# Performance work log

Hardware: AMD Instinct MI355X
Metric: run time of the kernel (lower is better)

## Reference

```python
import jax, jax.numpy as jnp
import numpy as np

NEG_SLOPE = 0.15
MASK_VAL = -1e9


def setup_inputs() -> dict:
    key = jax.random.key(0)
    k1, k2, k3, k4, k5 = jax.random.split(key, 5)
    B, N, D, H, QKV = 4, 1024, 128, 8, 16
    h = jax.random.normal(k1, (B, N, D), dtype=jnp.float32)
    same_cluster = jax.random.randint(k2, (B, N, N), 0, 2) > 0
    # nn.Linear weights stored as [in, out] (x @ W); scaled like default init
    Wa = jax.random.normal(k3, (2 * D + 1, H), dtype=jnp.float32) / np.sqrt(2 * D + 1)
    Wv = jax.random.normal(k4, (D, H * QKV), dtype=jnp.float32) / np.sqrt(D)
    Wo = jax.random.normal(k5, (H * QKV, D), dtype=jnp.float32) / np.sqrt(H * QKV)
    return {"h": h, "same_cluster": same_cluster, "Wa": Wa, "Wv": Wv, "Wo": Wo, "local_only": 0}


def reference(h, same_cluster, Wa, Wv, Wo, local_only):
    B, N, D = h.shape
    H = Wa.shape[1]
    # concat([hi, hj, edge]) @ Wa == hi @ Wa[:D] + hj @ Wa[D:2D] + edge * Wa[2D]
    Wa_i, Wa_j, w_e = Wa[:D], Wa[D:2 * D], Wa[2 * D]  # [D,H], [D,H], [H]
    s_i = h @ Wa_i  # [B, N, H]
    s_j = h @ Wa_j  # [B, N, H]
    edge = same_cluster.astype(h.dtype)  # [B, N, N]
    scores = s_i[:, :, None, :] + s_j[:, None, :, :] + edge[..., None] * w_e  # [B,N,N,H]
    scores = jax.nn.leaky_relu(scores, negative_slope=NEG_SLOPE)
    scores = jnp.moveaxis(scores, -1, 1)  # [B, H, N, N]
    if local_only:
        scores = jnp.where(same_cluster[:, None, :, :], scores, MASK_VAL)
    alpha = jax.nn.softmax(scores, axis=-1)  # [B, H, N, N]
    v = (h @ Wv).reshape(B, N, H, -1).transpose(0, 2, 1, 3)  # [B, H, N, qkv]
    out = jnp.einsum('bhij,bhjd->bhid', alpha, v)  # [B, H, N, qkv]
    out = out.transpose(0, 2, 1, 3).reshape(B, N, -1)  # [B, N, H*qkv]
    return out @ Wo  # [B, N, D]
```

## Files before the change

### kernel.cpp

```cpp
#include <hip/hip_runtime.h>
#include <hip/hip_bf16.h>


#define NEG_SLOPE 0.15f
#define B_ 4
#define N_ 1024
#define D_ 128
#define H_ 8
#define QKV_ 16
#define BN_ (B_ * N_)

__global__ __launch_bounds__(256) void prep_kernel(
    const float* __restrict__ h, const float* __restrict__ Wa,
    const float* __restrict__ Wv, float* __restrict__ SIt,
    float* __restrict__ SJt, float* __restrict__ V)
{
    __shared__ float hl[8][128];
    const int t  = threadIdx.x;
    const int R0 = blockIdx.x * 8;

    {
        const int f = t * 4;
        *(float4*)(&hl[0][0] + f) = *(const float4*)(h + R0 * 128 + f);
    }
    __syncthreads();

    const int cq = t & 31, rq = t >> 5;
    const int c4 = cq * 4;
    float acc0 = 0.f, acc1 = 0.f, acc2 = 0.f, acc3 = 0.f;
    #pragma unroll 8
    for (int k = 0; k < 128; ++k) {
        const float4 w = *(const float4*)(Wv + k * 128 + c4);
        const float a = hl[rq][k];
        acc0 += a * w.x; acc1 += a * w.y; acc2 += a * w.z; acc3 += a * w.w;
    }
    {
        const int R = R0 + rq, b = R >> 10, n = R & 1023;
        const int head = cq >> 2, dd = (cq & 3) * 4;
        float4 o; o.x = acc0; o.y = acc1; o.z = acc2; o.w = acc3;
        *(float4*)(V + ((size_t)(b * H_ + head) * N_ + n) * QKV_ + dd) = o;
    }

    {
        const int task = t >> 1, half = t & 1;
        const int row = task >> 4, which = (task >> 3) & 1, hh = task & 7;
        const float* wcol = Wa + which * 128 * H_ + hh;
        float s = 0.f;
        #pragma unroll 8
        for (int kk = 0; kk < 64; ++kk) {
            const int k = half * 64 + kk;
            s += hl[row][k] * wcol[k * H_];
        }
        s += __shfl_xor(s, 1, 64);
        if (!half) {
            float* dst = which ? SJt : SIt;
            dst[hh * BN_ + R0 + row] = s;
        }
    }
}

__global__ __launch_bounds__(256, 4) void attn_kernel(
    const float* __restrict__ SIt, const float* __restrict__ SJt,
    const float* __restrict__ V, const int* __restrict__ edge,
    const float* __restrict__ Wa, const int* __restrict__ local_only,
    float* __restrict__ ATT)
{
    const int t  = threadIdx.x;
    const int w  = t >> 6;
    const int l  = t & 63;
    const int hh = blockIdx.y;
    const int b  = blockIdx.z;
    const int i0 = blockIdx.x * 16 + w * 4;
    const int bn0 = b * N_;

    const float we = Wa[2 * D_ * H_ + hh];
    const int   lo = local_only[0];

    float si[4];
    #pragma unroll
    for (int r = 0; r < 4; ++r) si[r] = SIt[hh * BN_ + bn0 + i0 + r];

    const float* vbase  = V + (size_t)(b * H_ + hh) * N_ * QKV_;
    const float* sjbase = SJt + hh * BN_ + bn0;
    const int*   ebase  = edge + (size_t)(bn0 + i0) * N_;

    float acc[4][16];
    #pragma unroll
    for (int r = 0; r < 4; ++r)
        #pragma unroll
        for (int d = 0; d < 16; ++d) acc[r][d] = 0.f;
    float dsum[4] = {0.f, 0.f, 0.f, 0.f};

    #pragma unroll 2
    for (int j0 = 0; j0 < N_; j0 += 64) {
        const int j = j0 + l;
        const float sj = sjbase[j];
        const float4* vp = (const float4*)(vbase + j * QKV_);
        const float4 v0 = vp[0], v1 = vp[1], v2 = vp[2], v3 = vp[3];
        int e[4];
        #pragma unroll
        for (int r = 0; r < 4; ++r) e[r] = ebase[r * N_ + j];

        #pragma unroll
        for (int r = 0; r < 4; ++r) {
            float sc = si[r] + sj + (e[r] ? we : 0.f);
            sc = fmaxf(sc, NEG_SLOPE * sc);
            float p = __expf(sc);
            if (lo && !e[r]) p = 0.f;
            dsum[r] += p;
            acc[r][0]  += p * v0.x; acc[r][1]  += p * v0.y;
            acc[r][2]  += p * v0.z; acc[r][3]  += p * v0.w;
            acc[r][4]  += p * v1.x; acc[r][5]  += p * v1.y;
            acc[r][6]  += p * v1.z; acc[r][7]  += p * v1.w;
            acc[r][8]  += p * v2.x; acc[r][9]  += p * v2.y;
            acc[r][10] += p * v2.z; acc[r][11] += p * v2.w;
            acc[r][12] += p * v3.x; acc[r][13] += p * v3.y;
            acc[r][14] += p * v3.z; acc[r][15] += p * v3.w;
        }
    }

    const bool b3 = (l & 8) != 0;
    const bool b2 = (l & 4) != 0;
    const bool b1 = (l & 2) != 0;
    const bool b0 = (l & 1) != 0;
    float red[4];
    #pragma unroll
    for (int r = 0; r < 4; ++r) {
        float ds = dsum[r];
        #pragma unroll
        for (int m = 1; m < 64; m <<= 1) ds += __shfl_xor(ds, m, 64);
        dsum[r] = ds;

        float t8[8];
        #pragma unroll
        for (int d = 0; d < 8; ++d) {
            const float keep = b3 ? acc[r][d + 8] : acc[r][d];
            const float send = b3 ? acc[r][d]     : acc[r][d + 8];
            t8[d] = keep + __shfl_xor(send, 8, 64);
        }
        float t4[4];
        #pragma unroll
        for (int d = 0; d < 4; ++d) {
            const float keep = b2 ? t8[d + 4] : t8[d];
            const float send = b2 ? t8[d]     : t8[d + 4];
            t4[d] = keep + __shfl_xor(send, 4, 64);
        }
        float t2[2];
        #pragma unroll
        for (int d = 0; d < 2; ++d) {
            const float keep = b1 ? t4[d + 2] : t4[d];
            const float send = b1 ? t4[d]     : t4[d + 2];
            t2[d] = keep + __shfl_xor(send, 2, 64);
        }
        float t1;
        {
            const float keep = b0 ? t2[1] : t2[0];
            const float send = b0 ? t2[0] : t2[1];
            t1 = keep + __shfl_xor(send, 1, 64);
        }
        t1 += __shfl_xor(t1, 16, 64);
        t1 += __shfl_xor(t1, 32, 64);
        red[r] = t1;
    }

    {
        const int rsel = l >> 4;
        const float num = rsel == 0 ? red[0] : rsel == 1 ? red[1]
                        : rsel == 2 ? red[2] : red[3];
        const float den = rsel == 0 ? dsum[0] : rsel == 1 ? dsum[1]
                        : rsel == 2 ? dsum[2] : dsum[3];
        ATT[(size_t)(bn0 + i0 + rsel) * 128 + hh * 16 + (l & 15)] = num / den;
    }
}

__global__ __launch_bounds__(256) void out_kernel(
    const float* __restrict__ ATT, const float* __restrict__ Wo,
    float* __restrict__ out)
{
    __shared__ float al[8][128];
    const int t  = threadIdx.x;
    const int R0 = blockIdx.x * 8;
    {
        const int f = t * 4;
        *(float4*)(&al[0][0] + f) = *(const float4*)(ATT + (size_t)R0 * 128 + f);
    }
    __syncthreads();

    const int cq = t & 31, rq = t >> 5;
    const int c4 = cq * 4;
    float acc0 = 0.f, acc1 = 0.f, acc2 = 0.f, acc3 = 0.f;
    #pragma unroll 8
    for (int k = 0; k < 128; ++k) {
        const float4 w = *(const float4*)(Wo + k * 128 + c4);
        const float a = al[rq][k];
        acc0 += a * w.x; acc1 += a * w.y; acc2 += a * w.z; acc3 += a * w.w;
    }
    float4 o; o.x = acc0; o.y = acc1; o.z = acc2; o.w = acc3;
    *(float4*)(out + (size_t)(R0 + rq) * 128 + c4) = o;
}

extern "C" void kernel_launch(void* const* d_in, const int* in_sizes, int n_in,
                              void* d_out, int out_size, void* d_ws, size_t ws_size,
                              hipStream_t stream) {
    const float* h    = (const float*)d_in[0];
    const int*   edge = (const int*)d_in[1];
    const float* Wa   = (const float*)d_in[2];
    const float* Wv   = (const float*)d_in[3];
    const float* Wo   = (const float*)d_in[4];
    const int*   lo   = (const int*)d_in[5];
    float*       out  = (float*)d_out;

    float* ws  = (float*)d_ws;
    float* SIt = ws;
    float* SJt = SIt + H_ * BN_;
    float* V   = SJt + H_ * BN_;
    float* ATT = V + (size_t)B_ * H_ * N_ * QKV_;

    prep_kernel<<<BN_ / 8, 256, 0, stream>>>(h, Wa, Wv, SIt, SJt, V);
    attn_kernel<<<dim3(N_ / 16, H_, B_), 256, 0, stream>>>(SIt, SJt, V, edge, Wa, lo, ATT);
    out_kernel<<<BN_ / 8, 256, 0, stream>>>(ATT, Wo, out);
}
```

Measured before the change: 133.1 us.

## Use fp16 MFMA for attention-value product with transposed fp16 V

The attention kernel now computes the probability-times-V product with 16x16x32 fp16 MFMA instructions instead of scalar FMAs. V is stored transposed in fp16, scores are pre-scaled by log2(e) so exp2 can be used, and each wave handles a j-slice with partial results combined through shared memory. This removes the scalar FMA load and the long shuffle reduction. In exchange it adds fp16 rounding of probabilities and V, which can lose accuracy, plus an extra workspace memset.

Measured after the change: 125.1 us. 1.06x faster.

```diff
diff --git a/kernel.cpp b/kernel.cpp
--- a/kernel.cpp
+++ b/kernel.cpp
@@ -1,8 +1,10 @@
 #include <hip/hip_runtime.h>
 #include <hip/hip_bf16.h>
+#include <hip/hip_fp16.h>
 
 
 #define NEG_SLOPE 0.15f
+#define LOG2E 1.442695040888963f
 #define B_ 4
 #define N_ 1024
 #define D_ 128
@@ -10,10 +12,16 @@
 #define QKV_ 16
 #define BN_ (B_ * N_)
 
+typedef _Float16 half8 __attribute__((ext_vector_type(8)));
+typedef float f32x4 __attribute__((ext_vector_type(4)));
+
+#define WS_F32_COUNT (32768 + 32768 + 524288)
+#define WS_BYTES ((size_t)WS_F32_COUNT * 4 + (size_t)B_ * H_ * 16 * N_ * 2)
+
 __global__ __launch_bounds__(256) void prep_kernel(
     const float* __restrict__ h, const float* __restrict__ Wa,
     const float* __restrict__ Wv, float* __restrict__ SIt,
-    float* __restrict__ SJt, float* __restrict__ V)
+    float* __restrict__ SJt, _Float16* __restrict__ VT)
 {
     __shared__ float hl[8][128];
     const int t  = threadIdx.x;
@@ -21,24 +29,27 @@
 
     {
         const int f = t * 4;
-        *(float4*)(&hl[0][0] + f) = *(const float4*)(h + R0 * 128 + f);
+        *(float4*)(&hl[0][0] + f) = *(const float4*)(h + (size_t)R0 * 128 + f);
     }
     __syncthreads();
 
     const int cq = t & 31, rq = t >> 5;
     const int c4 = cq * 4;
-    float acc0 = 0.f, acc1 = 0.f, acc2 = 0.f, acc3 = 0.f;
+    float a0 = 0.f, a1 = 0.f, a2 = 0.f, a3 = 0.f;
     #pragma unroll 8
     for (int k = 0; k < 128; ++k) {
-        const float4 w = *(const float4*)(Wv + k * 128 + c4);
+        const float4 wv = *(const float4*)(Wv + k * 128 + c4);
         const float a = hl[rq][k];
-        acc0 += a * w.x; acc1 += a * w.y; acc2 += a * w.z; acc3 += a * w.w;
+        a0 += a * wv.x; a1 += a * wv.y; a2 += a * wv.z; a3 += a * wv.w;
     }
     {
         const int R = R0 + rq, b = R >> 10, n = R & 1023;
         const int head = cq >> 2, dd = (cq & 3) * 4;
-        float4 o; o.x = acc0; o.y = acc1; o.z = acc2; o.w = acc3;
-        *(float4*)(V + ((size_t)(b * H_ + head) * N_ + n) * QKV_ + dd) = o;
+        _Float16* vt = VT + ((size_t)(b * H_ + head) * 16 + dd) * N_ + n;
+        vt[0]      = (_Float16)a0;
+        vt[N_]     = (_Float16)a1;
+        vt[2 * N_] = (_Float16)a2;
+        vt[3 * N_] = (_Float16)a3;
     }
 
     {
@@ -54,122 +65,84 @@
         s += __shfl_xor(s, 1, 64);
         if (!half) {
             float* dst = which ? SJt : SIt;
-            dst[hh * BN_ + R0 + row] = s;
+            dst[hh * BN_ + R0 + row] = s * LOG2E;
         }
     }
 }
 
-__global__ __launch_bounds__(256, 4) void attn_kernel(
+__global__ __launch_bounds__(256) void attn_kernel(
     const float* __restrict__ SIt, const float* __restrict__ SJt,
-    const float* __restrict__ V, const int* __restrict__ edge,
+    const _Float16* __restrict__ VT, const int* __restrict__ edge,
     const float* __restrict__ Wa, const int* __restrict__ local_only,
     float* __restrict__ ATT)
 {
     const int t  = threadIdx.x;
     const int w  = t >> 6;
     const int l  = t & 63;
+    const int m  = l & 15;
+    const int kq = l >> 4;
     const int hh = blockIdx.y;
     const int b  = blockIdx.z;
-    const int i0 = blockIdx.x * 16 + w * 4;
+    const int i0 = blockIdx.x * 16;
     const int bn0 = b * N_;
 
-    const float we = Wa[2 * D_ * H_ + hh];
+    const float we = Wa[2 * D_ * H_ + hh] * LOG2E;
     const int   lo = local_only[0];
 
-    float si[4];
-    #pragma unroll
-    for (int r = 0; r < 4; ++r) si[r] = SIt[hh * BN_ + bn0 + i0 + r];
+    const float sim   = SIt[hh * BN_ + bn0 + i0 + m];
+    const float simwe = sim + we;
+    const float simNE = lo ? -1e6f : sim;
 
-    const float* vbase  = V + (size_t)(b * H_ + hh) * N_ * QKV_;
-    const float* sjbase = SJt + hh * BN_ + bn0;
-    const int*   ebase  = edge + (size_t)(bn0 + i0) * N_;
+    const float*    sjrow = SJt + hh * BN_ + bn0;
+    const int*      erow  = edge + (size_t)(bn0 + i0 + m) * N_;
+    const _Float16* vrow  = VT + ((size_t)(b * H_ + hh) * 16 + m) * N_;
 
-    float acc[4][16];
-    #pragma unroll
-    for (int r = 0; r < 4; ++r)
+    f32x4 acc = {0.f, 0.f, 0.f, 0.f};
+    float dsum = 0.f;
+
+    const int wj0 = w * 256;
+    #pragma unroll 2
+    for (int c = 0; c < 8; ++c) {
+        const int jb = wj0 + c * 32 + kq * 8;
+        const float4 sjA = *(const float4*)(sjrow + jb);
+        const float4 sjB = *(const float4*)(sjrow + jb + 4);
+        const int4   eA  = *(const int4*)(erow + jb);
+        const int4   eB  = *(const int4*)(erow + jb + 4);
+        const half8  bf  = *(const half8*)(vrow + jb);
+
+        const float sj[8] = {sjA.x, sjA.y, sjA.z, sjA.w,
+                             sjB.x, sjB.y, sjB.z, sjB.w};
+        const int   ee[8] = {eA.x, eA.y, eA.z, eA.w,
+                             eB.x, eB.y, eB.z, eB.w};
+        half8 av;
         #pragma unroll
-        for (int d = 0; d < 16; ++d) acc[r][d] = 0.f;
-    float dsum[4] = {0.f, 0.f, 0.f, 0.f};
-
-    #pragma unroll 2
-    for (int j0 = 0; j0 < N_; j0 += 64) {
-        const int j = j0 + l;
-        const float sj = sjbase[j];
-        const float4* vp = (const float4*)(vbase + j * QKV_);
-        const float4 v0 = vp[0], v1 = vp[1], v2 = vp[2], v3 = vp[3];
-        int e[4];
-        #pragma unroll
-        for (int r = 0; r < 4; ++r) e[r] = ebase[r * N_ + j];
-
-        #pragma unroll
-        for (int r = 0; r < 4; ++r) {
-            float sc = si[r] + sj + (e[r] ? we : 0.f);
-            sc = fmaxf(sc, NEG_SLOPE * sc);
-            float p = __expf(sc);
-            if (lo && !e[r]) p = 0.f;
-            dsum[r] += p;
-            acc[r][0]  += p * v0.x; acc[r][1]  += p * v0.y;
-            acc[r][2]  += p * v0.z; acc[r][3]  += p * v0.w;
-            acc[r][4]  += p * v1.x; acc[r][5]  += p * v1.y;
-            acc[r][6]  += p * v1.z; acc[r][7]  += p * v1.w;
-            acc[r][8]  += p * v2.x; acc[r][9]  += p * v2.y;
-            acc[r][10] += p * v2.z; acc[r][11] += p * v2.w;
-            acc[r][12] += p * v3.x; acc[r][13] += p * v3.y;
-            acc[r][14] += p * v3.z; acc[r][15] += p * v3.w;
+        for (int u = 0; u < 8; ++u) {
+            const float x  = (ee[u] ? simwe : simNE) + sj[u];
+            const float sc = fmaxf(x, NEG_SLOPE * x);
+            const float p  = exp2f(sc);
+            dsum += p;
+            av[u] = (_Float16)p;
         }
+        acc = __builtin_amdgcn_mfma_f32_16x16x32_f16(av, bf, acc, 0, 0, 0);
     }
 
-    const bool b3 = (l & 8) != 0;
-    const bool b2 = (l & 4) != 0;
-    const bool b1 = (l & 2) != 0;
-    const bool b0 = (l & 1) != 0;
-    float red[4];
+    dsum += __shfl_xor(dsum, 16, 64);
+    dsum += __shfl_xor(dsum, 32, 64);
+
+    __shared__ float olds[4][16][17];
+    __shared__ float denl[4][16];
     #pragma unroll
-    for (int r = 0; r < 4; ++r) {
-        float ds = dsum[r];
-        #pragma unroll
-        for (int m = 1; m < 64; m <<= 1) ds += __shfl_xor(ds, m, 64);
-        dsum[r] = ds;
-
-        float t8[8];
-        #pragma unroll
-        for (int d = 0; d < 8; ++d) {
-            const float keep = b3 ? acc[r][d + 8] : acc[r][d];
-            const float send = b3 ? acc[r][d]     : acc[r][d + 8];
-            t8[d] = keep + __shfl_xor(send, 8, 64);
-        }
-        float t4[4];
-        #pragma unroll
-        for (int d = 0; d < 4; ++d) {
-            const float keep = b2 ? t8[d + 4] : t8[d];
-            const float send = b2 ? t8[d]     : t8[d + 4];
-            t4[d] = keep + __shfl_xor(send, 4, 64);
-        }
-        float t2[2];
-        #pragma unroll
-        for (int d = 0; d < 2; ++d) {
-            const float keep = b1 ? t4[d + 2] : t4[d];
-            const float send = b1 ? t4[d]     : t4[d + 2];
-            t2[d] = keep + __shfl_xor(send, 2, 64);
-        }
-        float t1;
-        {
-            const float keep = b0 ? t2[1] : t2[0];
-            const float send = b0 ? t2[0] : t2[1];
-            t1 = keep + __shfl_xor(send, 1, 64);
-        }
-        t1 += __shfl_xor(t1, 16, 64);
-        t1 += __shfl_xor(t1, 32, 64);
-        red[r] = t1;
-    }
+    for (int reg = 0; reg < 4; ++reg)
+        olds[w][kq * 4 + reg][m] = acc[reg];
+    if (l < 16) denl[w][l] = dsum;
+    __syncthreads();
 
     {
-        const int rsel = l >> 4;
-        const float num = rsel == 0 ? red[0] : rsel == 1 ? red[1]
-                        : rsel == 2 ? red[2] : red[3];
-        const float den = rsel == 0 ? dsum[0] : rsel == 1 ? dsum[1]
-                        : rsel == 2 ? dsum[2] : dsum[3];
-        ATT[(size_t)(bn0 + i0 + rsel) * 128 + hh * 16 + (l & 15)] = num / den;
+        const int i = t >> 4, d = t & 15;
+        const float o   = olds[0][i][d] + olds[1][i][d]
+                        + olds[2][i][d] + olds[3][i][d];
+        const float den = denl[0][i] + denl[1][i] + denl[2][i] + denl[3][i];
+        ATT[(size_t)(bn0 + i0 + i) * 128 + hh * 16 + d] = o / den;
     }
 }
 
@@ -188,14 +161,14 @@
 
     const int cq = t & 31, rq = t >> 5;
     const int c4 = cq * 4;
-    float acc0 = 0.f, acc1 = 0.f, acc2 = 0.f, acc3 = 0.f;
+    float a0 = 0.f, a1 = 0.f, a2 = 0.f, a3 = 0.f;
     #pragma unroll 8
     for (int k = 0; k < 128; ++k) {
-        const float4 w = *(const float4*)(Wo + k * 128 + c4);
+        const float4 wv = *(const float4*)(Wo + k * 128 + c4);
         const float a = al[rq][k];
-        acc0 += a * w.x; acc1 += a * w.y; acc2 += a * w.z; acc3 += a * w.w;
+        a0 += a * wv.x; a1 += a * wv.y; a2 += a * wv.z; a3 += a * wv.w;
     }
-    float4 o; o.x = acc0; o.y = acc1; o.z = acc2; o.w = acc3;
+    float4 o; o.x = a0; o.y = a1; o.z = a2; o.w = a3;
     *(float4*)(out + (size_t)(R0 + rq) * 128 + c4) = o;
 }
 
@@ -210,13 +183,15 @@
     const int*   lo   = (const int*)d_in[5];
     float*       out  = (float*)d_out;
 
-    float* ws  = (float*)d_ws;
-    float* SIt = ws;
-    float* SJt = SIt + H_ * BN_;
-    float* V   = SJt + H_ * BN_;
-    float* ATT = V + (size_t)B_ * H_ * N_ * QKV_;
+    hipMemsetAsync(d_ws, 0, WS_BYTES, stream);
 
-    prep_kernel<<<BN_ / 8, 256, 0, stream>>>(h, Wa, Wv, SIt, SJt, V);
-    attn_kernel<<<dim3(N_ / 16, H_, B_), 256, 0, stream>>>(SIt, SJt, V, edge, Wa, lo, ATT);
+    float*     ws  = (float*)d_ws;
+    float*     SIt = ws;
+    float*     SJt = SIt + H_ * BN_;
+    float*     ATT = SJt + H_ * BN_;
+    _Float16*  VT  = (_Float16*)(ATT + (size_t)BN_ * 128);
+
+    prep_kernel<<<BN_ / 8, 256, 0, stream>>>(h, Wa, Wv, SIt, SJt, VT);
+    attn_kernel<<<dim3(N_ / 16, H_, B_), 256, 0, stream>>>(SIt, SJt, VT, edge, Wa, lo, ATT);
     out_kernel<<<BN_ / 8, 256, 0, stream>>>(ATT, Wo, out);
 }
```
